# Optimization experiments

Measured on AMD Instinct MI355X. Metric: run time of the kernel, lower is better.

The kernel has to match this reference:

```python
import jax, jax.numpy as jnp
import numpy as np

SEQ_LENGTH = 1000
NUM_FEATURES = 5
HIDDEN = 128


def setup_inputs() -> dict:
    key = jax.random.key(0)
    ks = jax.random.split(key, 12)
    k = 1.0 / np.sqrt(HIDDEN)  # torch default uniform bound
    # recurrence stays numerically bounded; math is identical.
    u = lambda kk, shape, s=k: jax.random.uniform(kk, shape, jnp.float32, -s, s)
    return {
        "x": jax.random.normal(ks[0], (256, 800, NUM_FEATURES), jnp.float32),
        "h_state": jnp.zeros((2, 256, HIDDEN), jnp.float32),
        "w_ih0": u(ks[1], (HIDDEN, NUM_FEATURES)),
        "w_hh0": u(ks[2], (HIDDEN, HIDDEN), 0.5 * k),
        "b_ih0": u(ks[3], (HIDDEN,)),
        "b_hh0": u(ks[4], (HIDDEN,)),
        "w_ih1": u(ks[5], (HIDDEN, HIDDEN), 0.5 * k),
        "w_hh1": u(ks[6], (HIDDEN, HIDDEN), 0.5 * k),
        "b_ih1": u(ks[7], (HIDDEN,)),
        "b_hh1": u(ks[8], (HIDDEN,)),
        "w_out": u(ks[9], (1, HIDDEN)),
        "b_out": u(ks[10], (1,)),
    }


def reference(x, h_state, w_ih0, w_hh0, b_ih0, b_hh0,
              w_ih1, w_hh1, b_ih1, b_hh1, w_out, b_out):
    B, T_in, F = x.shape
    # pad time dim to SEQ_LENGTH with zeros (torch.cat with delta)
    pad = jnp.zeros((B, SEQ_LENGTH - T_in, F), x.dtype)
    xp = jnp.concatenate([x, pad], axis=1)  # [B, 1000, F]
    xs = jnp.swapaxes(xp, 0, 1)  # [T, B, F] for scan

    def step(carry, x_t):
        h0, h1 = carry
        h0 = jax.nn.relu(x_t @ w_ih0.T + b_ih0 + h0 @ w_hh0.T + b_hh0)
        h1 = jax.nn.relu(h0 @ w_ih1.T + b_ih1 + h1 @ w_hh1.T + b_hh1)
        return (h0, h1), h1

    (h0f, h1f), ys = jax.lax.scan(step, (h_state[0], h_state[1]), xs)
    r_out = jnp.swapaxes(ys, 0, 1)  # [B, 1000, H]
    out = jax.nn.sigmoid(r_out @ w_out.T + b_out)  # [B, 1000, 1]
    return out[:, :T_in], jnp.stack([h0f, h1f])
```

## Files before the change

### kernel.cpp

```cpp
#include <hip/hip_runtime.h>
#include <math.h>


#define TT    1000
#define TIN   800
#define HD    128
#define NF    5
#define BATCH 256

typedef _Float16 h16x2 __attribute__((ext_vector_type(2)));
typedef _Float16 h16x8 __attribute__((ext_vector_type(8)));

template<int CTRL>
__device__ __forceinline__ float dpp_mov(float v) {
    union { float f; int i; } u, r;
    u.f = v;
    r.i = __builtin_amdgcn_update_dpp(0, u.i, CTRL, 0xF, 0xF, true);
    return r.f;
}

__global__ __launch_bounds__(768, 3) void rnn_dot2(
    const float* __restrict__ x,
    const float* __restrict__ h_state,
    const float* __restrict__ w_ih0,
    const float* __restrict__ w_hh0,
    const float* __restrict__ b_ih0,
    const float* __restrict__ b_hh0,
    const float* __restrict__ w_ih1,
    const float* __restrict__ w_hh1,
    const float* __restrict__ b_ih1,
    const float* __restrict__ b_hh1,
    const float* __restrict__ w_out,
    const float* __restrict__ b_out,
    float* __restrict__ out)
{
    __shared__ __align__(16) _Float16 x_h[TIN * 8];
    __shared__ __align__(16) _Float16 h0h[2][HD];
    __shared__ float A_f[2][HD];
    __shared__ __align__(16) _Float16 ring[32][HD];
    __shared__ float y_lds[TIN];

    const int tid = threadIdx.x;
    const int bb  = blockIdx.x;
    const int grp = tid >> 8;
    const int lt  = tid & 255;
    const int c   = lt & 15;
    const int rg  = lt >> 4;
    const int g   = (4 * (c & 1)) ^ (2 * ((c >> 1) & 1)) ^ (7 * ((c >> 2) & 1));
    const int row = rg * 8 + g;
    const bool writer = (c & 8) == 0;

    for (int i = tid; i < TIN * 8; i += 768) x_h[i] = (_Float16)0.f;
    __syncthreads();
    for (int i = tid; i < TIN * NF; i += 768) {
        int t = i / 5, f = i - 5 * t;
        x_h[t * 8 + f] = (_Float16)x[bb * (TIN * NF) + i];
    }
    if (tid < HD) {
        h0h[0][tid]  = (_Float16)h_state[bb * HD + tid];
        ring[31][tid] = (_Float16)h_state[BATCH * HD + bb * HD + tid];
    }

    const float* Wsrc = (grp == 0) ? w_hh0 : ((grp == 1) ? w_ih1 : w_hh1);
    h16x2 wp[8][4];
    #pragma unroll
    for (int j = 0; j < 8; ++j) {
        const float* rp = Wsrc + (rg * 8 + (j ^ g)) * HD + c * 8;
        #pragma unroll
        for (int t = 0; t < 4; ++t) {
            h16x2 w2 = { (_Float16)rp[2 * t], (_Float16)rp[2 * t + 1] };
            wp[j][t] = w2;
        }
    }
    h16x2 wx0 = {0,0}, wx1 = {0,0}, wx2 = {0,0};
    h16x2 wo[4];
    float bias = 0.f;
    if (grp == 0) {
        wx0[0] = (_Float16)w_ih0[row * NF + 0];
        wx0[1] = (_Float16)w_ih0[row * NF + 1];
        wx1[0] = (_Float16)w_ih0[row * NF + 2];
        wx1[1] = (_Float16)w_ih0[row * NF + 3];
        wx2[0] = (_Float16)w_ih0[row * NF + 4];
        bias = b_ih0[row] + b_hh0[row];
    } else if (grp == 1) {
        const int l4 = lt & 15;
        #pragma unroll
        for (int t = 0; t < 4; ++t) {
            wo[t][0] = (_Float16)w_out[l4 * 8 + 2 * t];
            wo[t][1] = (_Float16)w_out[l4 * 8 + 2 * t + 1];
        }
        bias = 0.f;
    } else {
        bias = b_ih1[row] + b_hh1[row];
    }
    const float bout = b_out[0];

    float hfin = 0.f;

    __syncthreads();

    auto matvec = [&](const _Float16* hbuf) -> float {
        h16x8 hv = *(const h16x8*)(hbuf + c * 8);
        h16x2 hp0 = { hv[0], hv[1] }, hp1 = { hv[2], hv[3] };
        h16x2 hp2 = { hv[4], hv[5] }, hp3 = { hv[6], hv[7] };
        float a[8];
        #pragma unroll
        for (int j = 0; j < 8; ++j) {
            float aj;
            aj = __builtin_amdgcn_fdot2(wp[j][0], hp0, 0.f, false);
            aj = __builtin_amdgcn_fdot2(wp[j][1], hp1, aj,  false);
            aj = __builtin_amdgcn_fdot2(wp[j][2], hp2, aj,  false);
            aj = __builtin_amdgcn_fdot2(wp[j][3], hp3, aj,  false);
            a[j] = aj;
        }
        a[0] += dpp_mov<0xB1>(a[4]);
        a[1] += dpp_mov<0xB1>(a[5]);
        a[2] += dpp_mov<0xB1>(a[6]);
        a[3] += dpp_mov<0xB1>(a[7]);
        a[0] += dpp_mov<0x4E>(a[2]);
        a[1] += dpp_mov<0x4E>(a[3]);
        a[0] += dpp_mov<0x140>(a[1]);
        a[0] += dpp_mov<0x128>(a[0]);
        return a[0];
    };

    #pragma unroll 2
    for (int s = 0; s < TT + 2; ++s) {
        const int p = s & 1;
        const int q = p ^ 1;

        if (grp == 0) {
            if (s < TT) {
                float acc = matvec(h0h[p]);
                float v = acc + bias;
                if (writer && s < TIN) {
                    h16x8 xv = *(const h16x8*)(&x_h[s * 8]);
                    h16x2 xp0 = { xv[0], xv[1] }, xp1 = { xv[2], xv[3] };
                    h16x2 xp2 = { xv[4], xv[5] };
                    float xc = __builtin_amdgcn_fdot2(wx2, xp2, 0.f, false);
                    xc = __builtin_amdgcn_fdot2(wx1, xp1, xc, false);
                    xc = __builtin_amdgcn_fdot2(wx0, xp0, xc, false);
                    v += xc;
                }
                v = fmaxf(v, 0.f);
                if (writer) {
                    h0h[q][row] = (_Float16)v;
                    if (s == TT - 1) hfin = v;
                }
            }
        } else if (grp == 1) {
            if (s <= TT) {
                float acc = matvec(h0h[p]);
                if (writer) A_f[q][row] = acc;
            }
            if (s >= 18 && s <= 818 && ((s - 2) & 15) == 0) {
                const int u  = (s - 33) + (lt >> 4);
                const int l4 = lt & 15;
                if (u >= 0 && u < TIN) {
                    h16x8 hv = *(const h16x8*)(&ring[u & 31][l4 * 8]);
                    h16x2 hp0 = { hv[0], hv[1] }, hp1 = { hv[2], hv[3] };
                    h16x2 hp2 = { hv[4], hv[5] }, hp3 = { hv[6], hv[7] };
                    float z;
                    z = __builtin_amdgcn_fdot2(wo[0], hp0, 0.f, false);
                    z = __builtin_amdgcn_fdot2(wo[1], hp1, z,  false);
                    z = __builtin_amdgcn_fdot2(wo[2], hp2, z,  false);
                    z = __builtin_amdgcn_fdot2(wo[3], hp3, z,  false);
                    z += dpp_mov<0xB1>(z);
                    z += dpp_mov<0x4E>(z);
                    z += dpp_mov<0x140>(z);
                    z += dpp_mov<0x128>(z);
                    if (l4 == 0) y_lds[u] = 1.f / (1.f + expf(-(z + bout)));
                }
            }
        } else {
            if (s >= 2) {
                const int u = s - 2;
                float acc = matvec(ring[(u + 31) & 31]);
                float pre = 0.f;
                if (writer) pre = A_f[p][row];
                float v = fmaxf(acc + bias + pre, 0.f);
                if (writer) {
                    ring[u & 31][row] = (_Float16)v;
                    if (u == TT - 1) hfin = v;
                }
            }
        }
        __syncthreads();
    }

    for (int i = tid; i < TIN; i += 768)
        out[bb * TIN + i] = y_lds[i];
    if (grp == 0 && writer)
        out[TIN * BATCH + bb * HD + row] = hfin;
    if (grp == 2 && writer)
        out[TIN * BATCH + BATCH * HD + bb * HD + row] = hfin;
}

extern "C" void kernel_launch(void* const* d_in, const int* in_sizes, int n_in,
                              void* d_out, int out_size, void* d_ws, size_t ws_size,
                              hipStream_t stream) {
    (void)in_sizes; (void)n_in; (void)d_ws; (void)ws_size; (void)out_size;
    rnn_dot2<<<dim3(BATCH), dim3(768), 0, stream>>>(
        (const float*)d_in[0],  (const float*)d_in[1],
        (const float*)d_in[2],  (const float*)d_in[3],
        (const float*)d_in[4],  (const float*)d_in[5],
        (const float*)d_in[6],  (const float*)d_in[7],
        (const float*)d_in[8],  (const float*)d_in[9],
        (const float*)d_in[10], (const float*)d_in[11],
        (float*)d_out);
}
```

Baseline: 503.2 us.

## Shrink RNN block to four waves with one wave per matvec stage

The work split changes from three 256-thread groups to one 64-lane wave per stage: the layer-0 recurrence, the layer-1 input projection, the layer-1 recurrence, and the output head. Each lane now holds 8 rows by 32 columns of weights (128 fp16 pairs in registers) and produces two outputs, so the cross-lane reduction drops from four DPP steps to two. The aim is to cut per-step barrier and synchronisation cost with a 256-thread block. In exchange each lane runs four times more dot2 instructions per step on the serial critical path, and the larger register footprint may limit occupancy.

```diff
diff --git a/kernel.cpp b/kernel.cpp
--- a/kernel.cpp
+++ b/kernel.cpp
@@ -19,7 +19,7 @@
     return r.f;
 }
 
-__global__ __launch_bounds__(768, 3) void rnn_dot2(
+__global__ __launch_bounds__(256, 1) void rnn_w4(
     const float* __restrict__ x,
     const float* __restrict__ h_state,
     const float* __restrict__ w_ih0,
@@ -36,81 +36,96 @@
 {
     __shared__ __align__(16) _Float16 x_h[TIN * 8];
     __shared__ __align__(16) _Float16 h0h[2][HD];
-    __shared__ float A_f[2][HD];
+    __shared__ __align__(16) float A_f[2][HD];
     __shared__ __align__(16) _Float16 ring[32][HD];
     __shared__ float y_lds[TIN];
 
-    const int tid = threadIdx.x;
-    const int bb  = blockIdx.x;
-    const int grp = tid >> 8;
-    const int lt  = tid & 255;
-    const int c   = lt & 15;
-    const int rg  = lt >> 4;
-    const int g   = (4 * (c & 1)) ^ (2 * ((c >> 1) & 1)) ^ (7 * ((c >> 2) & 1));
-    const int row = rg * 8 + g;
-    const bool writer = (c & 8) == 0;
-
-    for (int i = tid; i < TIN * 8; i += 768) x_h[i] = (_Float16)0.f;
+    const int tid  = threadIdx.x;
+    const int bb   = blockIdx.x;
+    const int wv   = tid >> 6;
+    const int lane = tid & 63;
+    const int c    = lane & 3;
+    const int rg   = lane >> 2;
+    const int g    = 4 * (c & 1) + 2 * ((c >> 1) & 1);
+    const int base = rg * 8 + g;
+
+    for (int i = tid; i < TIN * 8; i += 256) x_h[i] = (_Float16)0.f;
     __syncthreads();
-    for (int i = tid; i < TIN * NF; i += 768) {
+    for (int i = tid; i < TIN * NF; i += 256) {
         int t = i / 5, f = i - 5 * t;
         x_h[t * 8 + f] = (_Float16)x[bb * (TIN * NF) + i];
     }
     if (tid < HD) {
-        h0h[0][tid]  = (_Float16)h_state[bb * HD + tid];
+        h0h[0][tid]   = (_Float16)h_state[bb * HD + tid];
         ring[31][tid] = (_Float16)h_state[BATCH * HD + bb * HD + tid];
     }
 
-    const float* Wsrc = (grp == 0) ? w_hh0 : ((grp == 1) ? w_ih1 : w_hh1);
-    h16x2 wp[8][4];
-    #pragma unroll
-    for (int j = 0; j < 8; ++j) {
-        const float* rp = Wsrc + (rg * 8 + (j ^ g)) * HD + c * 8;
-        #pragma unroll
-        for (int t = 0; t < 4; ++t) {
-            h16x2 w2 = { (_Float16)rp[2 * t], (_Float16)rp[2 * t + 1] };
-            wp[j][t] = w2;
-        }
-    }
-    h16x2 wx0 = {0,0}, wx1 = {0,0}, wx2 = {0,0};
-    h16x2 wo[4];
-    float bias = 0.f;
-    if (grp == 0) {
-        wx0[0] = (_Float16)w_ih0[row * NF + 0];
-        wx0[1] = (_Float16)w_ih0[row * NF + 1];
-        wx1[0] = (_Float16)w_ih0[row * NF + 2];
-        wx1[1] = (_Float16)w_ih0[row * NF + 3];
-        wx2[0] = (_Float16)w_ih0[row * NF + 4];
-        bias = b_ih0[row] + b_hh0[row];
-    } else if (grp == 1) {
-        const int l4 = lt & 15;
-        #pragma unroll
-        for (int t = 0; t < 4; ++t) {
-            wo[t][0] = (_Float16)w_out[l4 * 8 + 2 * t];
-            wo[t][1] = (_Float16)w_out[l4 * 8 + 2 * t + 1];
-        }
-        bias = 0.f;
-    } else {
-        bias = b_ih1[row] + b_hh1[row];
+    h16x2 wp[8][16];
+    if (wv < 3) {
+        const float* Wsrc = (wv == 0) ? w_hh0 : ((wv == 1) ? w_ih1 : w_hh1);
+        #pragma unroll
+        for (int j = 0; j < 8; ++j) {
+            const float* rp = Wsrc + (rg * 8 + (j ^ g)) * HD + c * 32;
+            #pragma unroll
+            for (int t = 0; t < 16; ++t) {
+                h16x2 w2 = { (_Float16)rp[2 * t], (_Float16)rp[2 * t + 1] };
+                wp[j][t] = w2;
+            }
+        }
+    }
+
+    h16x2 wxa[3], wxb[3];
+    h16x2 wo[16];
+    float bias0 = 0.f, bias1 = 0.f;
+    if (wv == 0) {
+        #pragma unroll
+        for (int k = 0; k < 3; ++k) {
+            _Float16 a0 = (_Float16)w_ih0[base * NF + 2 * k];
+            _Float16 a1 = (2 * k + 1 < NF) ? (_Float16)w_ih0[base * NF + 2 * k + 1] : (_Float16)0.f;
+            _Float16 b0 = (_Float16)w_ih0[(base + 1) * NF + 2 * k];
+            _Float16 b1 = (2 * k + 1 < NF) ? (_Float16)w_ih0[(base + 1) * NF + 2 * k + 1] : (_Float16)0.f;
+            h16x2 wa = { a0, a1 }; wxa[k] = wa;
+            h16x2 wb = { b0, b1 }; wxb[k] = wb;
+        }
+        bias0 = b_ih0[base] + b_hh0[base];
+        bias1 = b_ih0[base + 1] + b_hh0[base + 1];
+    } else if (wv == 2) {
+        bias0 = b_ih1[base] + b_hh1[base];
+        bias1 = b_ih1[base + 1] + b_hh1[base + 1];
+    } else if (wv == 3) {
+        #pragma unroll
+        for (int t = 0; t < 16; ++t) {
+            h16x2 w2 = { (_Float16)w_out[c * 32 + 2 * t],
+                         (_Float16)w_out[c * 32 + 2 * t + 1] };
+            wo[t] = w2;
+        }
     }
     const float bout = b_out[0];
 
-    float hfin = 0.f;
+    float hfin0 = 0.f, hfin1 = 0.f;
 
     __syncthreads();
 
-    auto matvec = [&](const _Float16* hbuf) -> float {
-        h16x8 hv = *(const h16x8*)(hbuf + c * 8);
-        h16x2 hp0 = { hv[0], hv[1] }, hp1 = { hv[2], hv[3] };
-        h16x2 hp2 = { hv[4], hv[5] }, hp3 = { hv[6], hv[7] };
+    auto matvec = [&](const _Float16* hbuf, float& r0, float& r1) {
+        h16x8 hv[4];
+        #pragma unroll
+        for (int u2 = 0; u2 < 4; ++u2)
+            hv[u2] = *(const h16x8*)(hbuf + c * 32 + 8 * u2);
         float a[8];
         #pragma unroll
         for (int j = 0; j < 8; ++j) {
-            float aj;
-            aj = __builtin_amdgcn_fdot2(wp[j][0], hp0, 0.f, false);
-            aj = __builtin_amdgcn_fdot2(wp[j][1], hp1, aj,  false);
-            aj = __builtin_amdgcn_fdot2(wp[j][2], hp2, aj,  false);
-            aj = __builtin_amdgcn_fdot2(wp[j][3], hp3, aj,  false);
+            float aj = 0.f;
+            #pragma unroll
+            for (int u2 = 0; u2 < 4; ++u2) {
+                h16x2 hp0 = { hv[u2][0], hv[u2][1] };
+                h16x2 hp1 = { hv[u2][2], hv[u2][3] };
+                h16x2 hp2 = { hv[u2][4], hv[u2][5] };
+                h16x2 hp3 = { hv[u2][6], hv[u2][7] };
+                aj = __builtin_amdgcn_fdot2(wp[j][4 * u2 + 0], hp0, aj, false);
+                aj = __builtin_amdgcn_fdot2(wp[j][4 * u2 + 1], hp1, aj, false);
+                aj = __builtin_amdgcn_fdot2(wp[j][4 * u2 + 2], hp2, aj, false);
+                aj = __builtin_amdgcn_fdot2(wp[j][4 * u2 + 3], hp3, aj, false);
+            }
             a[j] = aj;
         }
         a[0] += dpp_mov<0xB1>(a[4]);
@@ -119,9 +134,8 @@
         a[3] += dpp_mov<0xB1>(a[7]);
         a[0] += dpp_mov<0x4E>(a[2]);
         a[1] += dpp_mov<0x4E>(a[3]);
-        a[0] += dpp_mov<0x140>(a[1]);
-        a[0] += dpp_mov<0x128>(a[0]);
-        return a[0];
+        r0 = a[0];
+        r1 = a[1];
     };
 
     #pragma unroll 2
@@ -129,78 +143,89 @@
         const int p = s & 1;
         const int q = p ^ 1;
 
-        if (grp == 0) {
+        if (wv == 0) {
             if (s < TT) {
-                float acc = matvec(h0h[p]);
-                float v = acc + bias;
-                if (writer && s < TIN) {
+                float v0, v1;
+                matvec(h0h[p], v0, v1);
+                v0 += bias0; v1 += bias1;
+                if (s < TIN) {
                     h16x8 xv = *(const h16x8*)(&x_h[s * 8]);
-                    h16x2 xp0 = { xv[0], xv[1] }, xp1 = { xv[2], xv[3] };
+                    h16x2 xp0 = { xv[0], xv[1] };
+                    h16x2 xp1 = { xv[2], xv[3] };
                     h16x2 xp2 = { xv[4], xv[5] };
-                    float xc = __builtin_amdgcn_fdot2(wx2, xp2, 0.f, false);
-                    xc = __builtin_amdgcn_fdot2(wx1, xp1, xc, false);
-                    xc = __builtin_amdgcn_fdot2(wx0, xp0, xc, false);
-                    v += xc;
+                    float xc0 = __builtin_amdgcn_fdot2(wxa[2], xp2, 0.f, false);
+                    xc0 = __builtin_amdgcn_fdot2(wxa[1], xp1, xc0, false);
+                    xc0 = __builtin_amdgcn_fdot2(wxa[0], xp0, xc0, false);
+                    float xc1 = __builtin_amdgcn_fdot2(wxb[2], xp2, 0.f, false);
+                    xc1 = __builtin_amdgcn_fdot2(wxb[1], xp1, xc1, false);
+                    xc1 = __builtin_amdgcn_fdot2(wxb[0], xp0, xc1, false);
+                    v0 += xc0; v1 += xc1;
                 }
-                v = fmaxf(v, 0.f);
-                if (writer) {
-                    h0h[q][row] = (_Float16)v;
-                    if (s == TT - 1) hfin = v;
-                }
-            }
-        } else if (grp == 1) {
+                v0 = fmaxf(v0, 0.f);
+                v1 = fmaxf(v1, 0.f);
+                h16x2 hv = { (_Float16)v0, (_Float16)v1 };
+                *(h16x2*)(&h0h[q][base]) = hv;
+                if (s == TT - 1) { hfin0 = v0; hfin1 = v1; }
+            }
+        } else if (wv == 1) {
             if (s <= TT) {
-                float acc = matvec(h0h[p]);
-                if (writer) A_f[q][row] = acc;
-            }
+                float v0, v1;
+                matvec(h0h[p], v0, v1);
+                *(float2*)(&A_f[q][base]) = make_float2(v0, v1);
+            }
+        } else if (wv == 2) {
+            if (s >= 2) {
+                const int u = s - 2;
+                float v0, v1;
+                matvec(&ring[(u + 31) & 31][0], v0, v1);
+                float2 av = *(const float2*)(&A_f[p][base]);
+                v0 = fmaxf(v0 + bias0 + av.x, 0.f);
+                v1 = fmaxf(v1 + bias1 + av.y, 0.f);
+                h16x2 hv = { (_Float16)v0, (_Float16)v1 };
+                *(h16x2*)(&ring[u & 31][base]) = hv;
+                if (u == TT - 1) { hfin0 = v0; hfin1 = v1; }
+            }
+        } else {
             if (s >= 18 && s <= 818 && ((s - 2) & 15) == 0) {
-                const int u  = (s - 33) + (lt >> 4);
-                const int l4 = lt & 15;
+                const int slot = lane >> 2;
+                const int u    = (s - 33) + slot;
                 if (u >= 0 && u < TIN) {
-                    h16x8 hv = *(const h16x8*)(&ring[u & 31][l4 * 8]);
-                    h16x2 hp0 = { hv[0], hv[1] }, hp1 = { hv[2], hv[3] };
-                    h16x2 hp2 = { hv[4], hv[5] }, hp3 = { hv[6], hv[7] };
-                    float z;
-                    z = __builtin_amdgcn_fdot2(wo[0], hp0, 0.f, false);
-                    z = __builtin_amdgcn_fdot2(wo[1], hp1, z,  false);
-                    z = __builtin_amdgcn_fdot2(wo[2], hp2, z,  false);
-                    z = __builtin_amdgcn_fdot2(wo[3], hp3, z,  false);
+                    const _Float16* rb = &ring[u & 31][0] + c * 32;
+                    float z = 0.f;
+                    #pragma unroll
+                    for (int u2 = 0; u2 < 4; ++u2) {
+                        h16x8 hv = *(const h16x8*)(rb + 8 * u2);
+                        h16x2 hp0 = { hv[0], hv[1] };
+                        h16x2 hp1 = { hv[2], hv[3] };
+                        h16x2 hp2 = { hv[4], hv[5] };
+                        h16x2 hp3 = { hv[6], hv[7] };
+                        z = __builtin_amdgcn_fdot2(wo[4 * u2 + 0], hp0, z, false);
+                        z = __builtin_amdgcn_fdot2(wo[4 * u2 + 1], hp1, z, false);
+                        z = __builtin_amdgcn_fdot2(wo[4 * u2 + 2], hp2, z, false);
+                        z = __builtin_amdgcn_fdot2(wo[4 * u2 + 3], hp3, z, false);
+                    }
                     z += dpp_mov<0xB1>(z);
                     z += dpp_mov<0x4E>(z);
-                    z += dpp_mov<0x140>(z);
-                    z += dpp_mov<0x128>(z);
-                    if (l4 == 0) y_lds[u] = 1.f / (1.f + expf(-(z + bout)));
+                    if (c == 0) y_lds[u] = 1.f / (1.f + expf(-(z + bout)));
                 }
             }
-        } else {
-            if (s >= 2) {
-                const int u = s - 2;
-                float acc = matvec(ring[(u + 31) & 31]);
-                float pre = 0.f;
-                if (writer) pre = A_f[p][row];
-                float v = fmaxf(acc + bias + pre, 0.f);
-                if (writer) {
-                    ring[u & 31][row] = (_Float16)v;
-                    if (u == TT - 1) hfin = v;
-                }
-            }
         }
         __syncthreads();
     }
 
-    for (int i = tid; i < TIN; i += 768)
+    for (int i = tid; i < TIN; i += 256)
         out[bb * TIN + i] = y_lds[i];
-    if (grp == 0 && writer)
-        out[TIN * BATCH + bb * HD + row] = hfin;
-    if (grp == 2 && writer)
-        out[TIN * BATCH + BATCH * HD + bb * HD + row] = hfin;
+    if (wv == 0)
+        *(float2*)(&out[TIN * BATCH + bb * HD + base]) = make_float2(hfin0, hfin1);
+    if (wv == 2)
+        *(float2*)(&out[TIN * BATCH + BATCH * HD + bb * HD + base]) = make_float2(hfin0, hfin1);
 }
 
 extern "C" void kernel_launch(void* const* d_in, const int* in_sizes, int n_in,
                               void* d_out, int out_size, void* d_ws, size_t ws_size,
                               hipStream_t stream) {
     (void)in_sizes; (void)n_in; (void)d_ws; (void)ws_size; (void)out_size;
-    rnn_dot2<<<dim3(BATCH), dim3(768), 0, stream>>>(
+    rnn_w4<<<dim3(BATCH), dim3(256), 0, stream>>>(
         (const float*)d_in[0],  (const float*)d_in[1],
         (const float*)d_in[2],  (const float*)d_in[3],
         (const float*)d_in[4],  (const float*)d_in[5],
```

New measurement: 511.3 us. No clear change (+1.6%).
